# Optimization experiments

Measured on AMD Instinct MI355X. Metric: run time of the kernel, lower is better.

The kernel has to match this reference:

```python
import jax, jax.numpy as jnp
import numpy as np

N = 50000   # nodes
E = 800000  # edges
F = 128     # input features
H = 128     # hidden channels
G = 64      # graphs in batch
C = 10      # classes
L_HID = 3   # residual hidden GCN blocks
EPS = 1e-5  # BatchNorm eps


def setup_inputs() -> dict:
    key = jax.random.key(0)
    ks = jax.random.split(key, 10)
    sc = lambda k, s: (jax.random.normal(k, s, jnp.float32) * 0.05)
    x = jax.random.normal(ks[0], (N, F), jnp.float32)
    edge_index = jax.random.randint(ks[1], (2, E), 0, N, dtype=jnp.int32)
    batch = jnp.sort(jax.random.randint(ks[2], (N,), 0, G, dtype=jnp.int32))
    return {
        "x": x, "edge_index": edge_index, "batch": batch,
        # initial GCN block
        "W0": sc(ks[3], (F, H)), "b0": jnp.zeros(H, jnp.float32),
        "g0": jnp.ones(H, jnp.float32), "be0": jnp.zeros(H, jnp.float32),
        # 3 residual GCN blocks (stacked)
        "Wh": sc(ks[4], (L_HID, H, H)), "bh": jnp.zeros((L_HID, H), jnp.float32),
        "gh": jnp.ones((L_HID, H), jnp.float32), "beh": jnp.zeros((L_HID, H), jnp.float32),
        "Rh": sc(ks[5], (L_HID, H, H)),  # residual Linear (no bias)
        # MLP head: Linear(H,H)+ReLU, Linear(H,C)
        "mW1": sc(ks[6], (H, H)), "mb1": jnp.zeros(H, jnp.float32),
        "mW2": sc(ks[7], (H, C)), "mb2": jnp.zeros(C, jnp.float32),
    }


def _gcn_norm(edge_index, n):
    # add self-loops + symmetric normalization, as in PyG GCNConv
    loop = jnp.arange(n, dtype=edge_index.dtype)
    src = jnp.concatenate([edge_index[0], loop])
    dst = jnp.concatenate([edge_index[1], loop])
    deg = jax.ops.segment_sum(jnp.ones_like(dst, jnp.float32), dst, num_segments=n)
    dinv = jnp.where(deg > 0, jax.lax.rsqrt(deg), 0.0)
    coef = dinv[src] * dinv[dst]  # [E+N]
    return src, dst, coef


def _gcn_conv(x, W, b, src, dst, coef, n):
    h = x @ W                                   # [N, H] linear first (PyG order)
    msg = h[src] * coef[:, None]                # gather + normalize  [E+N, H]
    agg = jax.ops.segment_sum(msg, dst, num_segments=n)  # scatter-add [N, H]
    return agg + b


def _bn_relu(h, gamma, beta):
    # BatchNorm1d in eval mode with running_mean=0, running_var=1
    inv = jax.lax.rsqrt(jnp.asarray(1.0 + EPS, h.dtype))
    return jax.nn.relu(h * inv * gamma + beta)  # dropout is identity in eval


def reference(x, edge_index, batch, W0, b0, g0, be0, Wh, bh, gh, beh, Rh, mW1, mb1, mW2, mb2):
    n = x.shape[0]
    src, dst, coef = _gcn_norm(edge_index, n)
    # initial block (no residual)
    h = _bn_relu(_gcn_conv(x, W0, b0, src, dst, coef, n), g0, be0)
    # residual hidden blocks
    for i in range(Wh.shape[0]):
        c = _gcn_conv(h, Wh[i], bh[i], src, dst, coef, n) + h @ Rh[i]
        h = _bn_relu(c, gh[i], beh[i])
    # global max pool over graphs in the batch
    pooled = jax.ops.segment_max(h, batch, num_segments=G)  # [G, H]
    # MLP head
    z = jax.nn.relu(pooled @ mW1 + mb1)
    return z @ mW2 + mb2  # [G, C]
```

## Files before the change

kernel.cpp:

```cpp
#include <hip/hip_runtime.h>
#include <cstdint>
#include <cstddef>

#define NN 50000
#define NE 800000
#define NEPAD (NE + 3 * NN)
#define HID 128
#define NGRAPH 64
#define NCLASS 10
#define LHID 3
#define NREP 8

#define ROWBLK 3125
#define ROWBLK_PAD 3128
#define GEMM_GRID 782
#define FILL_GRID 3125
#define FRONT_DEG 3125
#define FRONT_A 3125
#define FRONT_B 56
#define FRONT_GRID (FRONT_DEG + FRONT_A + FRONT_B)

static constexpr float BN_INV = 0.9999950000374996f;

typedef __attribute__((ext_vector_type(8))) __bf16 bf16x8;
typedef __attribute__((ext_vector_type(4))) float floatx4;


__device__ __forceinline__ unsigned int f32_to_bf16_rne(float f) {
    unsigned int u = __float_as_uint(f);
    return (u + 0x7FFFu + ((u >> 16) & 1u)) >> 16;
}
__device__ __forceinline__ float bf16_to_f32(unsigned int h) {
    return __uint_as_float(h << 16);
}
__device__ __forceinline__ void split2(float a, float b, unsigned int& hi,
                                       unsigned int& lo) {
    unsigned int h0 = f32_to_bf16_rne(a), h1 = f32_to_bf16_rne(b);
    unsigned int l0 = f32_to_bf16_rne(a - bf16_to_f32(h0));
    unsigned int l1 = f32_to_bf16_rne(b - bf16_to_f32(h1));
    hi = h0 | (h1 << 16);
    lo = l0 | (l1 << 16);
}

__device__ __forceinline__ void gl2lds16(const void* g, void* l) {
    __builtin_amdgcn_global_load_lds((__attribute__((address_space(1))) void*)g,
                                     (__attribute__((address_space(3))) void*)l,
                                     16, 0, 0);
}


__global__ void k_front(const float* __restrict__ x, unsigned short* __restrict__ xH,
                        unsigned short* __restrict__ xL,
                        const float* __restrict__ W0, const float* __restrict__ Wh,
                        const float* __restrict__ Rh, unsigned short* __restrict__ bH,
                        unsigned short* __restrict__ bL,
                        const int* __restrict__ ei, int* __restrict__ deg8,
                        int* __restrict__ eslot) {
    const int b = blockIdx.x;
    const int tid = threadIdx.x;
    if (b < FRONT_DEG) {
        int e = b * 256 + tid;
        int d = ei[NE + e];
        int rep = e & (NREP - 1);
        eslot[e] = atomicAdd(&deg8[rep * NN + d], 1);
    } else if (b < FRONT_DEG + FRONT_A) {
        int u = (b - FRONT_DEG) * 256 + tid;
        int lane = u & 63;
        int blk = u >> 6;
        int kblk = blk & 3;
        int rowBlock = blk >> 2;
        int m = rowBlock * 16 + (lane & 15);
        int k = kblk * 32 + (lane >> 4) * 8;
        const float4* p = (const float4*)&x[(size_t)m * 128 + k];
        float4 v0 = p[0];
        float4 v1 = p[1];
        float vals[8] = {v0.x, v0.y, v0.z, v0.w, v1.x, v1.y, v1.z, v1.w};
        union { unsigned int i[4]; uint4 v; } H, L;
#pragma unroll
        for (int j = 0; j < 4; ++j) split2(vals[2 * j], vals[2 * j + 1], H.i[j], L.i[j]);
        *(uint4*)&xH[(size_t)u * 8] = H.v;
        *(uint4*)&xL[(size_t)u * 8] = L.v;
    } else {
        int cb = b - FRONT_DEG - FRONT_A;
        int mat = cb >> 3;
        const float* src = (mat == 0) ? W0
                         : (mat <= 3) ? (Wh + (size_t)(mat - 1) * 16384)
                                      : (Rh + (size_t)(mat - 4) * 16384);
        int u = (cb & 7) * 256 + tid;
        int lane = u & 63;
        int blk = u >> 6;
        int kblk = blk & 3;
        int nb = blk >> 2;
        int n = nb * 16 + (lane & 15);
        int k = kblk * 32 + (lane >> 4) * 8;
        union { unsigned int i[4]; uint4 v; } H, L;
#pragma unroll
        for (int j = 0; j < 4; ++j) {
            float a = src[(size_t)(k + 2 * j) * 128 + n];
            float c = src[(size_t)(k + 2 * j + 1) * 128 + n];
            split2(a, c, H.i[j], L.i[j]);
        }
        size_t base = (size_t)mat * 16384 + (size_t)u * 8;
        *(uint4*)&bH[base] = H.v;
        *(uint4*)&bL[base] = L.v;
    }
}


__global__ void k_scan1(const int* __restrict__ deg8, int* __restrict__ degT,
                        int* __restrict__ degOff, float* __restrict__ dinv,
                        int* __restrict__ bsum) {
    __shared__ int s[256];
    int i = blockIdx.x * 256 + threadIdx.x;
    int dsum = 0;
    if (i < NN) {
        int off[NREP];
#pragma unroll
        for (int r = 0; r < NREP; ++r) {
            off[r] = dsum;
            dsum += deg8[r * NN + i];
        }
#pragma unroll
        for (int r = 0; r < NREP; ++r) degOff[i * NREP + r] = off[r];
        degT[i] = dsum;
        dinv[i] = rsqrtf((float)(dsum + 1));
    }
    s[threadIdx.x] = (dsum + 3) & ~3;
    __syncthreads();
    for (int o = 128; o > 0; o >>= 1) {
        if (threadIdx.x < o) s[threadIdx.x] += s[threadIdx.x + o];
        __syncthreads();
    }
    if (threadIdx.x == 0) bsum[blockIdx.x] = s[0];
}


__global__ void k_scan3(const int* __restrict__ degT, const int* __restrict__ bsum,
                        int* __restrict__ rowptr, int* __restrict__ col,
                        float* __restrict__ cfv) {
    __shared__ int s[256];
    __shared__ int offS;
    const int bid = blockIdx.x;
    s[threadIdx.x] = (threadIdx.x < bid) ? bsum[threadIdx.x] : 0;
    __syncthreads();
    for (int o = 128; o > 0; o >>= 1) {
        if (threadIdx.x < o) s[threadIdx.x] += s[threadIdx.x + o];
        __syncthreads();
    }
    if (threadIdx.x == 0) offS = s[0];
    __syncthreads();
    const int off = offS;
    __syncthreads();
    int i = bid * 256 + threadIdx.x;
    int d = (i < NN) ? degT[i] : 0;
    int v = (d + 3) & ~3;
    s[threadIdx.x] = v;
    __syncthreads();
    for (int o = 1; o < 256; o <<= 1) {
        int tv = (threadIdx.x >= o) ? s[threadIdx.x - o] : 0;
        __syncthreads();
        s[threadIdx.x] += tv;
        __syncthreads();
    }
    if (i < NN) {
        int rp = off + s[threadIdx.x] - v;
        rowptr[i] = rp;
        for (int p = rp + d; p < rp + v; ++p) { col[p] = 0; cfv[p] = 0.f; }
    }
}


template <int NB, bool FILL>
__global__ __launch_bounds__(256, 3) void k_gemm_mfma(
    const unsigned short* __restrict__ Ahi, const unsigned short* __restrict__ Alo,
    const unsigned short* __restrict__ B1hi, const unsigned short* __restrict__ B1lo,
    const unsigned short* __restrict__ B2hi, const unsigned short* __restrict__ B2lo,
    float* __restrict__ C1, float* __restrict__ C2,
    const int* __restrict__ ei, const int* __restrict__ rowptr,
    const int* __restrict__ eslot, const int* __restrict__ degOff,
    const float* __restrict__ dinv, int* __restrict__ col,
    float* __restrict__ cfv) {
    __shared__ unsigned short lds[(1 + 2 * NB) * 4096];
    if (FILL && blockIdx.x >= GEMM_GRID) {
        int e = (blockIdx.x - GEMM_GRID) * 256 + threadIdx.x;
        int s = ei[e];
        int d = ei[NE + e];
        int rep = e & (NREP - 1);
        int p = rowptr[d] + degOff[d * NREP + rep] + eslot[e];
        col[p] = s;
        cfv[p] = dinv[s];
        return;
    }
    unsigned short* AhiS = lds;
    unsigned short* AloS = lds + 2048;
    unsigned short* B1hiS = lds + 4096;
    unsigned short* B1loS = lds + 8192;
    unsigned short* B2hiS = lds + 12288;
    unsigned short* B2loS = lds + 16384;

    const int tid = threadIdx.x;
    const int wave = tid >> 6;
    const int lane = tid & 63;
    const int wm = wave & 1;
    const int wn = wave >> 1;
    const int rb0 = blockIdx.x * 4;

    floatx4 acc1[2][4], acc2[2][4];
    floatx4 zero = {0.f, 0.f, 0.f, 0.f};
#pragma unroll
    for (int i = 0; i < 2; ++i)
#pragma unroll
        for (int j = 0; j < 4; ++j) { acc1[i][j] = zero; if (NB == 2) acc2[i][j] = zero; }

    for (int kc = 0; kc < 4; ++kc) {
        const int nit = (NB == 2) ? 10 : 6;
#pragma unroll
        for (int it = 0; it < nit; ++it) {
            int i = it * 4 + wave;
            const unsigned short* src;
            unsigned short* dst;
            if (i < 4)       { src = Ahi  + ((size_t)(rb0 + i) * 4 + kc) * 512;       dst = AhiS  + i * 512; }
            else if (i < 8)  { int rb = i - 4;  src = Alo  + ((size_t)(rb0 + rb) * 4 + kc) * 512; dst = AloS  + rb * 512; }
            else if (i < 16) { int nb = i - 8;  src = B1hi + ((size_t)nb * 4 + kc) * 512;         dst = B1hiS + nb * 512; }
            else if (i < 24) { int nb = i - 16; src = B1lo + ((size_t)nb * 4 + kc) * 512;         dst = B1loS + nb * 512; }
            else if (i < 32) { int nb = i - 24; src = B2hi + ((size_t)nb * 4 + kc) * 512;         dst = B2hiS + nb * 512; }
            else             { int nb = i - 32; src = B2lo + ((size_t)nb * 4 + kc) * 512;         dst = B2loS + nb * 512; }
            gl2lds16(src + (size_t)lane * 8, dst);
        }
        __syncthreads();

        bf16x8 aH[2], aL[2], bH[4], bL[4];
#pragma unroll
        for (int t = 0; t < 2; ++t)
            aH[t] = *(const bf16x8*)(AhiS + (wm * 2 + t) * 512 + lane * 8);
#pragma unroll
        for (int t = 0; t < 4; ++t)
            bH[t] = *(const bf16x8*)(B1hiS + (wn * 4 + t) * 512 + lane * 8);
#pragma unroll
        for (int tm = 0; tm < 2; ++tm)
#pragma unroll
            for (int tn = 0; tn < 4; ++tn)
                acc1[tm][tn] = __builtin_amdgcn_mfma_f32_16x16x32_bf16(
                    aH[tm], bH[tn], acc1[tm][tn], 0, 0, 0);
#pragma unroll
        for (int t = 0; t < 4; ++t)
            bL[t] = *(const bf16x8*)(B1loS + (wn * 4 + t) * 512 + lane * 8);
#pragma unroll
        for (int tm = 0; tm < 2; ++tm)
#pragma unroll
            for (int tn = 0; tn < 4; ++tn)
                acc1[tm][tn] = __builtin_amdgcn_mfma_f32_16x16x32_bf16(
                    aH[tm], bL[tn], acc1[tm][tn], 0, 0, 0);
#pragma unroll
        for (int t = 0; t < 2; ++t)
            aL[t] = *(const bf16x8*)(AloS + (wm * 2 + t) * 512 + lane * 8);
#pragma unroll
        for (int tm = 0; tm < 2; ++tm)
#pragma unroll
            for (int tn = 0; tn < 4; ++tn)
                acc1[tm][tn] = __builtin_amdgcn_mfma_f32_16x16x32_bf16(
                    aL[tm], bH[tn], acc1[tm][tn], 0, 0, 0);
        if (NB == 2) {
#pragma unroll
            for (int t = 0; t < 4; ++t)
                bH[t] = *(const bf16x8*)(B2hiS + (wn * 4 + t) * 512 + lane * 8);
#pragma unroll
            for (int tm = 0; tm < 2; ++tm)
#pragma unroll
                for (int tn = 0; tn < 4; ++tn)
                    acc2[tm][tn] = __builtin_amdgcn_mfma_f32_16x16x32_bf16(
                        aH[tm], bH[tn], acc2[tm][tn], 0, 0, 0);
#pragma unroll
            for (int tm = 0; tm < 2; ++tm)
#pragma unroll
                for (int tn = 0; tn < 4; ++tn)
                    acc2[tm][tn] = __builtin_amdgcn_mfma_f32_16x16x32_bf16(
                        aL[tm], bH[tn], acc2[tm][tn], 0, 0, 0);
#pragma unroll
            for (int t = 0; t < 4; ++t)
                bL[t] = *(const bf16x8*)(B2loS + (wn * 4 + t) * 512 + lane * 8);
#pragma unroll
            for (int tm = 0; tm < 2; ++tm)
#pragma unroll
                for (int tn = 0; tn < 4; ++tn)
                    acc2[tm][tn] = __builtin_amdgcn_mfma_f32_16x16x32_bf16(
                        aH[tm], bL[tn], acc2[tm][tn], 0, 0, 0);
        }
        __syncthreads();
    }

    const int quad = lane >> 4;
    const int col0 = lane & 15;
    const int rowBase = blockIdx.x * 64 + wm * 32;
#pragma unroll
    for (int tm = 0; tm < 2; ++tm) {
#pragma unroll
        for (int tn = 0; tn < 4; ++tn) {
            int c = wn * 64 + tn * 16 + col0;
#pragma unroll
            for (int r = 0; r < 4; ++r) {
                int row = rowBase + tm * 16 + quad * 4 + r;
                if (row < NN) {
                    C1[(size_t)row * 128 + c] = acc1[tm][tn][r];
                    if (NB == 2) C2[(size_t)row * 128 + c] = acc2[tm][tn][r];
                }
            }
        }
    }
}


template <bool RES, bool LAST>
__global__ __launch_bounds__(1024, 8) void k_spmm(
    const float* __restrict__ t, const float* __restrict__ r,
    const int* __restrict__ rowptr, const int* __restrict__ degT,
    const int* __restrict__ col, const float* __restrict__ cfv,
    const float* __restrict__ dinv, const float* __restrict__ bias,
    const float* __restrict__ gamma, const float* __restrict__ beta,
    unsigned short* __restrict__ hHi, unsigned short* __restrict__ hLo,
    const int* __restrict__ batch, float* __restrict__ pooled) {
    __shared__ unsigned short shH[16][136];
    __shared__ unsigned short shL[16][136];
    __shared__ float shP[16][128];
    const int tid = threadIdx.x;
    const int lane = tid & 63;
    const int h = lane >> 5;
    const int f4 = lane & 31;
    const int wv = __builtin_amdgcn_readfirstlane(tid >> 6);
    const int node = blockIdx.x * 16 + wv;

    const int start = __builtin_amdgcn_readfirstlane(rowptr[node]);
    const int cnt4 = __builtin_amdgcn_readfirstlane((degT[node] + 3) >> 2);

    float4 acc = {0.f, 0.f, 0.f, 0.f};
#pragma unroll 4
    for (int q = 0; q < cnt4; ++q) {
        const int4 cs = *(const int4*)(col + start + q * 4);
        const float4 wvv = *(const float4*)(cfv + start + q * 4);
        const int rowA = h ? cs.y : cs.x;
        const int rowB = h ? cs.w : cs.z;
        const float wA = h ? wvv.y : wvv.x;
        const float wB = h ? wvv.w : wvv.z;
        const float4 vA = *(const float4*)&t[(size_t)rowA * 128 + f4 * 4];
        const float4 vB = *(const float4*)&t[(size_t)rowB * 128 + f4 * 4];
        acc.x = fmaf(wA, vA.x, acc.x); acc.y = fmaf(wA, vA.y, acc.y);
        acc.z = fmaf(wA, vA.z, acc.z); acc.w = fmaf(wA, vA.w, acc.w);
        acc.x = fmaf(wB, vB.x, acc.x); acc.y = fmaf(wB, vB.y, acc.y);
        acc.z = fmaf(wB, vB.z, acc.z); acc.w = fmaf(wB, vB.w, acc.w);
    }
    acc.x += __shfl_xor(acc.x, 32);
    acc.y += __shfl_xor(acc.y, 32);
    acc.z += __shfl_xor(acc.z, 32);
    acc.w += __shfl_xor(acc.w, 32);

    const int f0 = f4 * 4;
    float4 o;
    if (h == 0) {
        const float di = dinv[node];
        const float dii = di * di;
        const float4 tv = *(const float4*)&t[(size_t)node * 128 + f0];
        const float4 bv = *(const float4*)&bias[f0];
        const float4 gv = *(const float4*)&gamma[f0];
        const float4 ev = *(const float4*)&beta[f0];
        float4 cc;
        cc.x = di * acc.x + dii * tv.x + bv.x;
        cc.y = di * acc.y + dii * tv.y + bv.y;
        cc.z = di * acc.z + dii * tv.z + bv.z;
        cc.w = di * acc.w + dii * tv.w + bv.w;
        if (RES) {
            const float4 rv = *(const float4*)&r[(size_t)node * 128 + f0];
            cc.x += rv.x; cc.y += rv.y; cc.z += rv.z; cc.w += rv.w;
        }
        o.x = fmaxf(cc.x * (BN_INV * gv.x) + ev.x, 0.f);
        o.y = fmaxf(cc.y * (BN_INV * gv.y) + ev.y, 0.f);
        o.z = fmaxf(cc.z * (BN_INV * gv.z) + ev.z, 0.f);
        o.w = fmaxf(cc.w * (BN_INV * gv.w) + ev.w, 0.f);
    }

    if (LAST) {
        bool uni = (batch[blockIdx.x * 16] == batch[blockIdx.x * 16 + 15]);
        if (uni) {
            if (h == 0) *(float4*)&shP[wv][f0] = o;
            __syncthreads();
            if (wv == 0) {
                float a = shP[0][2 * lane], b = shP[0][2 * lane + 1];
#pragma unroll
                for (int w = 1; w < 16; ++w) {
                    a = fmaxf(a, shP[w][2 * lane]);
                    b = fmaxf(b, shP[w][2 * lane + 1]);
                }
                int g = batch[blockIdx.x * 16];
                atomicMax((unsigned int*)&pooled[g * 128 + 2 * lane],
                          __float_as_uint(a));
                atomicMax((unsigned int*)&pooled[g * 128 + 2 * lane + 1],
                          __float_as_uint(b));
            }
        } else if (h == 0) {
            int g = batch[node];
            atomicMax((unsigned int*)&pooled[g * 128 + f0], __float_as_uint(o.x));
            atomicMax((unsigned int*)&pooled[g * 128 + f0 + 1], __float_as_uint(o.y));
            atomicMax((unsigned int*)&pooled[g * 128 + f0 + 2], __float_as_uint(o.z));
            atomicMax((unsigned int*)&pooled[g * 128 + f0 + 3], __float_as_uint(o.w));
        }
        return;
    }

    if (h == 0) {
        unsigned int H0, L0, H1, L1;
        split2(o.x, o.y, H0, L0);
        split2(o.z, o.w, H1, L1);
        ((unsigned int*)&shH[wv][0])[f4 * 2] = H0;
        ((unsigned int*)&shH[wv][0])[f4 * 2 + 1] = H1;
        ((unsigned int*)&shL[wv][0])[f4 * 2] = L0;
        ((unsigned int*)&shL[wv][0])[f4 * 2 + 1] = L1;
    }
    __syncthreads();

    const int u = tid >> 6;
    const int l = tid & 63;
    const int m = l & 15;
    const int kg = l >> 4;
    if (u < 4) {
        uint4 H4 = *(const uint4*)&shH[m][u * 32 + kg * 8];
        ((uint4*)hHi)[((size_t)blockIdx.x * 4 + u) * 64 + l] = H4;
    } else if (u < 8) {
        int uu = u - 4;
        uint4 L4 = *(const uint4*)&shL[m][uu * 32 + kg * 8];
        ((uint4*)hLo)[((size_t)blockIdx.x * 4 + uu) * 64 + l] = L4;
    }
}


__global__ void k_head(const float* __restrict__ pooled, const float* __restrict__ mW1,
                       const float* __restrict__ mb1, const float* __restrict__ mW2,
                       const float* __restrict__ mb2, float* __restrict__ out) {
    __shared__ float p[128];
    __shared__ float z[128];
    int g = blockIdx.x;
    int j = threadIdx.x;
    p[j] = pooled[g * 128 + j];
    __syncthreads();
    float a = mb1[j];
#pragma unroll 8
    for (int k = 0; k < 128; ++k) a += p[k] * mW1[k * 128 + j];
    z[j] = fmaxf(a, 0.f);
    __syncthreads();
    if (j < NCLASS) {
        float o = mb2[j];
#pragma unroll 8
        for (int k = 0; k < 128; ++k) o += z[k] * mW2[k * NCLASS + j];
        out[g * NCLASS + j] = o;
    }
}


extern "C" void kernel_launch(void* const* d_in, const int* in_sizes, int n_in,
                              void* d_out, int out_size, void* d_ws, size_t ws_size,
                              hipStream_t stream) {
    const float* x   = (const float*)d_in[0];
    const int*   ei  = (const int*)d_in[1];
    const int* batch = (const int*)d_in[2];
    const float* W0  = (const float*)d_in[3];
    const float* b0  = (const float*)d_in[4];
    const float* g0  = (const float*)d_in[5];
    const float* be0 = (const float*)d_in[6];
    const float* Wh  = (const float*)d_in[7];
    const float* bh  = (const float*)d_in[8];
    const float* gh  = (const float*)d_in[9];
    const float* beh = (const float*)d_in[10];
    const float* Rh  = (const float*)d_in[11];
    const float* mW1 = (const float*)d_in[12];
    const float* mb1 = (const float*)d_in[13];
    const float* mW2 = (const float*)d_in[14];
    const float* mb2 = (const float*)d_in[15];
    float* out = (float*)d_out;

    char* ws = (char*)d_ws;
    size_t off = 0;
    auto alloc = [&](size_t bytes) -> void* {
        void* p = ws + off;
        off += (bytes + 255) & ~(size_t)255;
        return p;
    };
    int*   deg8   = (int*)alloc((size_t)NREP * NN * 4);
    float* pooled = (float*)alloc((size_t)NGRAPH * HID * 4);
    size_t zspan = (size_t)((char*)pooled - (char*)deg8) + (size_t)NGRAPH * HID * 4;
    int*   degT   = (int*)alloc((size_t)NN * 4);
    int*   degOff = (int*)alloc((size_t)NN * NREP * 4);
    int*   rowptr = (int*)alloc((size_t)NN * 4);
    float* dinv   = (float*)alloc((size_t)NN * 4);
    int*   bsum   = (int*)alloc(256 * 4);
    int*   eslot  = (int*)alloc((size_t)NE * 4);
    int*   col    = (int*)alloc((size_t)NEPAD * 4);
    float* cfv    = (float*)alloc((size_t)NEPAD * 4);
    float* t      = (float*)alloc((size_t)NN * HID * 4);
    float* rbuf   = (float*)alloc((size_t)NN * HID * 4);
    const size_t ASZ = (size_t)ROWBLK_PAD * 4 * 512;
    unsigned short* xH = (unsigned short*)alloc(ASZ * 2);
    unsigned short* xL = (unsigned short*)alloc(ASZ * 2);
    unsigned short* hH0 = (unsigned short*)alloc(ASZ * 2);
    unsigned short* hL0 = (unsigned short*)alloc(ASZ * 2);
    unsigned short* hH1 = (unsigned short*)alloc(ASZ * 2);
    unsigned short* hL1 = (unsigned short*)alloc(ASZ * 2);
    unsigned short* bH = (unsigned short*)alloc((size_t)7 * 16384 * 2);
    unsigned short* bL = (unsigned short*)alloc((size_t)7 * 16384 * 2);

    hipMemsetAsync(deg8, 0, zspan, stream);

    k_front<<<FRONT_GRID, 256, 0, stream>>>(x, xH, xL, W0, Wh, Rh, bH, bL,
                                            ei, deg8, eslot);
    k_scan1<<<(NN + 255) / 256, 256, 0, stream>>>(deg8, degT, degOff, dinv, bsum);
    k_scan3<<<(NN + 255) / 256, 256, 0, stream>>>(degT, bsum, rowptr, col, cfv);

    k_gemm_mfma<1, true><<<GEMM_GRID + FILL_GRID, 256, 0, stream>>>(
        xH, xL, bH, bL, nullptr, nullptr, t, nullptr,
        ei, rowptr, eslot, degOff, dinv, col, cfv);

    const int spmmGrid = NN / 16;
    k_spmm<false, false><<<spmmGrid, 1024, 0, stream>>>(
        t, nullptr, rowptr, degT, col, cfv, dinv, b0, g0, be0, hH0, hL0,
        nullptr, nullptr);

    unsigned short* hh[2] = {hH0, hH1};
    unsigned short* hl[2] = {hL0, hL1};
    int cur = 0;
    for (int i = 0; i < LHID; ++i) {
        unsigned short* ih = hh[cur];
        unsigned short* il = hl[cur];
        unsigned short* oh = hh[cur ^ 1];
        unsigned short* ol = hl[cur ^ 1];
        const unsigned short* w1H = bH + (size_t)(1 + i) * 16384;
        const unsigned short* w1L = bL + (size_t)(1 + i) * 16384;
        const unsigned short* w2H = bH + (size_t)(4 + i) * 16384;
        const unsigned short* w2L = bL + (size_t)(4 + i) * 16384;
        k_gemm_mfma<2, false><<<GEMM_GRID, 256, 0, stream>>>(
            ih, il, w1H, w1L, w2H, w2L, t, rbuf,
            nullptr, nullptr, nullptr, nullptr, nullptr, nullptr, nullptr);
        if (i < LHID - 1)
            k_spmm<true, false><<<spmmGrid, 1024, 0, stream>>>(
                t, rbuf, rowptr, degT, col, cfv, dinv, bh + i * HID, gh + i * HID,
                beh + i * HID, oh, ol, nullptr, nullptr);
        else
            k_spmm<true, true><<<spmmGrid, 1024, 0, stream>>>(
                t, rbuf, rowptr, degT, col, cfv, dinv, bh + i * HID, gh + i * HID,
                beh + i * HID, nullptr, nullptr, batch, pooled);
        cur ^= 1;
    }

    k_head<<<NGRAPH, 128, 0, stream>>>(pooled, mW1, mb1, mW2, mb2, out);
}
```

Before: 497.6 us.

## Fuse x bf16 split into first GEMM and load operands directly to registers

The separate pass that converts x into hi/lo bf16 tiles in the front kernel is removed. The first GEMM now reads fp32 x and splits it in registers. Separately, the GEMM drops its LDS staging and block barriers, loading A and B fragments straight from global memory into registers. This saves the x round-trip through memory and the sync overhead, at the cost of redundant global reads of B across waves and no shared-memory reuse.

```diff
diff --git a/kernel.cpp b/kernel.cpp
--- a/kernel.cpp
+++ b/kernel.cpp
@@ -16,9 +16,8 @@
 #define GEMM_GRID 782
 #define FILL_GRID 3125
 #define FRONT_DEG 3125
-#define FRONT_A 3125
 #define FRONT_B 56
-#define FRONT_GRID (FRONT_DEG + FRONT_A + FRONT_B)
+#define FRONT_GRID (FRONT_DEG + FRONT_B)
 
 static constexpr float BN_INV = 0.9999950000374996f;
 
@@ -42,16 +41,8 @@
     lo = l0 | (l1 << 16);
 }
 
-__device__ __forceinline__ void gl2lds16(const void* g, void* l) {
-    __builtin_amdgcn_global_load_lds((__attribute__((address_space(1))) void*)g,
-                                     (__attribute__((address_space(3))) void*)l,
-                                     16, 0, 0);
-}
-
-
-__global__ void k_front(const float* __restrict__ x, unsigned short* __restrict__ xH,
-                        unsigned short* __restrict__ xL,
-                        const float* __restrict__ W0, const float* __restrict__ Wh,
+
+__global__ void k_front(const float* __restrict__ W0, const float* __restrict__ Wh,
                         const float* __restrict__ Rh, unsigned short* __restrict__ bH,
                         unsigned short* __restrict__ bL,
                         const int* __restrict__ ei, int* __restrict__ deg8,
@@ -63,25 +54,8 @@
         int d = ei[NE + e];
         int rep = e & (NREP - 1);
         eslot[e] = atomicAdd(&deg8[rep * NN + d], 1);
-    } else if (b < FRONT_DEG + FRONT_A) {
-        int u = (b - FRONT_DEG) * 256 + tid;
-        int lane = u & 63;
-        int blk = u >> 6;
-        int kblk = blk & 3;
-        int rowBlock = blk >> 2;
-        int m = rowBlock * 16 + (lane & 15);
-        int k = kblk * 32 + (lane >> 4) * 8;
-        const float4* p = (const float4*)&x[(size_t)m * 128 + k];
-        float4 v0 = p[0];
-        float4 v1 = p[1];
-        float vals[8] = {v0.x, v0.y, v0.z, v0.w, v1.x, v1.y, v1.z, v1.w};
-        union { unsigned int i[4]; uint4 v; } H, L;
-#pragma unroll
-        for (int j = 0; j < 4; ++j) split2(vals[2 * j], vals[2 * j + 1], H.i[j], L.i[j]);
-        *(uint4*)&xH[(size_t)u * 8] = H.v;
-        *(uint4*)&xL[(size_t)u * 8] = L.v;
     } else {
-        int cb = b - FRONT_DEG - FRONT_A;
+        int cb = b - FRONT_DEG;
         int mat = cb >> 3;
         const float* src = (mat == 0) ? W0
                          : (mat <= 3) ? (Wh + (size_t)(mat - 1) * 16384)
@@ -170,8 +144,9 @@
 }
 
 
-template <int NB, bool FILL>
+template <int NB, bool FILL, bool XA>
 __global__ __launch_bounds__(256, 3) void k_gemm_mfma(
+    const float* __restrict__ X,
     const unsigned short* __restrict__ Ahi, const unsigned short* __restrict__ Alo,
     const unsigned short* __restrict__ B1hi, const unsigned short* __restrict__ B1lo,
     const unsigned short* __restrict__ B2hi, const unsigned short* __restrict__ B2lo,
@@ -180,7 +155,6 @@
     const int* __restrict__ eslot, const int* __restrict__ degOff,
     const float* __restrict__ dinv, int* __restrict__ col,
     float* __restrict__ cfv) {
-    __shared__ unsigned short lds[(1 + 2 * NB) * 4096];
     if (FILL && blockIdx.x >= GEMM_GRID) {
         int e = (blockIdx.x - GEMM_GRID) * 256 + threadIdx.x;
         int s = ei[e];
@@ -191,13 +165,6 @@
         cfv[p] = dinv[s];
         return;
     }
-    unsigned short* AhiS = lds;
-    unsigned short* AloS = lds + 2048;
-    unsigned short* B1hiS = lds + 4096;
-    unsigned short* B1loS = lds + 8192;
-    unsigned short* B2hiS = lds + 12288;
-    unsigned short* B2loS = lds + 16384;
-
     const int tid = threadIdx.x;
     const int wave = tid >> 6;
     const int lane = tid & 63;
@@ -212,30 +179,38 @@
 #pragma unroll
         for (int j = 0; j < 4; ++j) { acc1[i][j] = zero; if (NB == 2) acc2[i][j] = zero; }
 
+#pragma unroll
     for (int kc = 0; kc < 4; ++kc) {
-        const int nit = (NB == 2) ? 10 : 6;
-#pragma unroll
-        for (int it = 0; it < nit; ++it) {
-            int i = it * 4 + wave;
-            const unsigned short* src;
-            unsigned short* dst;
-            if (i < 4)       { src = Ahi  + ((size_t)(rb0 + i) * 4 + kc) * 512;       dst = AhiS  + i * 512; }
-            else if (i < 8)  { int rb = i - 4;  src = Alo  + ((size_t)(rb0 + rb) * 4 + kc) * 512; dst = AloS  + rb * 512; }
-            else if (i < 16) { int nb = i - 8;  src = B1hi + ((size_t)nb * 4 + kc) * 512;         dst = B1hiS + nb * 512; }
-            else if (i < 24) { int nb = i - 16; src = B1lo + ((size_t)nb * 4 + kc) * 512;         dst = B1loS + nb * 512; }
-            else if (i < 32) { int nb = i - 24; src = B2hi + ((size_t)nb * 4 + kc) * 512;         dst = B2hiS + nb * 512; }
-            else             { int nb = i - 32; src = B2lo + ((size_t)nb * 4 + kc) * 512;         dst = B2loS + nb * 512; }
-            gl2lds16(src + (size_t)lane * 8, dst);
-        }
-        __syncthreads();
-
         bf16x8 aH[2], aL[2], bH[4], bL[4];
-#pragma unroll
-        for (int t = 0; t < 2; ++t)
-            aH[t] = *(const bf16x8*)(AhiS + (wm * 2 + t) * 512 + lane * 8);
+        if (XA) {
+#pragma unroll
+            for (int t = 0; t < 2; ++t) {
+                int m = (rb0 + wm * 2 + t) * 16 + (lane & 15);
+                if (m >= NN) m = NN - 1;
+                const float4* p =
+                    (const float4*)&X[(size_t)m * 128 + kc * 32 + (lane >> 4) * 8];
+                float4 v0 = p[0];
+                float4 v1 = p[1];
+                float vals[8] = {v0.x, v0.y, v0.z, v0.w, v1.x, v1.y, v1.z, v1.w};
+                union { unsigned int i[4]; bf16x8 v; } H, L;
+#pragma unroll
+                for (int j = 0; j < 4; ++j)
+                    split2(vals[2 * j], vals[2 * j + 1], H.i[j], L.i[j]);
+                aH[t] = H.v;
+                aL[t] = L.v;
+            }
+        } else {
+#pragma unroll
+            for (int t = 0; t < 2; ++t) {
+                size_t u = ((size_t)(rb0 + wm * 2 + t) * 4 + kc) * 512 + lane * 8;
+                aH[t] = *(const bf16x8*)(Ahi + u);
+                aL[t] = *(const bf16x8*)(Alo + u);
+            }
+        }
 #pragma unroll
         for (int t = 0; t < 4; ++t)
-            bH[t] = *(const bf16x8*)(B1hiS + (wn * 4 + t) * 512 + lane * 8);
+            bH[t] = *(const bf16x8*)(B1hi + ((size_t)(wn * 4 + t) * 4 + kc) * 512 +
+                                     lane * 8);
 #pragma unroll
         for (int tm = 0; tm < 2; ++tm)
 #pragma unroll
@@ -244,16 +219,14 @@
                     aH[tm], bH[tn], acc1[tm][tn], 0, 0, 0);
 #pragma unroll
         for (int t = 0; t < 4; ++t)
-            bL[t] = *(const bf16x8*)(B1loS + (wn * 4 + t) * 512 + lane * 8);
+            bL[t] = *(const bf16x8*)(B1lo + ((size_t)(wn * 4 + t) * 4 + kc) * 512 +
+                                     lane * 8);
 #pragma unroll
         for (int tm = 0; tm < 2; ++tm)
 #pragma unroll
             for (int tn = 0; tn < 4; ++tn)
                 acc1[tm][tn] = __builtin_amdgcn_mfma_f32_16x16x32_bf16(
                     aH[tm], bL[tn], acc1[tm][tn], 0, 0, 0);
-#pragma unroll
-        for (int t = 0; t < 2; ++t)
-            aL[t] = *(const bf16x8*)(AloS + (wm * 2 + t) * 512 + lane * 8);
 #pragma unroll
         for (int tm = 0; tm < 2; ++tm)
 #pragma unroll
@@ -263,7 +236,8 @@
         if (NB == 2) {
 #pragma unroll
             for (int t = 0; t < 4; ++t)
-                bH[t] = *(const bf16x8*)(B2hiS + (wn * 4 + t) * 512 + lane * 8);
+                bH[t] = *(const bf16x8*)(B2hi + ((size_t)(wn * 4 + t) * 4 + kc) * 512 +
+                                         lane * 8);
 #pragma unroll
             for (int tm = 0; tm < 2; ++tm)
 #pragma unroll
@@ -278,7 +252,8 @@
                         aL[tm], bH[tn], acc2[tm][tn], 0, 0, 0);
 #pragma unroll
             for (int t = 0; t < 4; ++t)
-                bL[t] = *(const bf16x8*)(B2loS + (wn * 4 + t) * 512 + lane * 8);
+                bL[t] = *(const bf16x8*)(B2lo + ((size_t)(wn * 4 + t) * 4 + kc) * 512 +
+                                         lane * 8);
 #pragma unroll
             for (int tm = 0; tm < 2; ++tm)
 #pragma unroll
@@ -286,7 +261,6 @@
                     acc2[tm][tn] = __builtin_amdgcn_mfma_f32_16x16x32_bf16(
                         aH[tm], bL[tn], acc2[tm][tn], 0, 0, 0);
         }
-        __syncthreads();
     }
 
     const int quad = lane >> 4;
@@ -496,8 +470,6 @@
     float* t      = (float*)alloc((size_t)NN * HID * 4);
     float* rbuf   = (float*)alloc((size_t)NN * HID * 4);
     const size_t ASZ = (size_t)ROWBLK_PAD * 4 * 512;
-    unsigned short* xH = (unsigned short*)alloc(ASZ * 2);
-    unsigned short* xL = (unsigned short*)alloc(ASZ * 2);
     unsigned short* hH0 = (unsigned short*)alloc(ASZ * 2);
     unsigned short* hL0 = (unsigned short*)alloc(ASZ * 2);
     unsigned short* hH1 = (unsigned short*)alloc(ASZ * 2);
@@ -507,13 +479,12 @@
 
     hipMemsetAsync(deg8, 0, zspan, stream);
 
-    k_front<<<FRONT_GRID, 256, 0, stream>>>(x, xH, xL, W0, Wh, Rh, bH, bL,
-                                            ei, deg8, eslot);
+    k_front<<<FRONT_GRID, 256, 0, stream>>>(W0, Wh, Rh, bH, bL, ei, deg8, eslot);
     k_scan1<<<(NN + 255) / 256, 256, 0, stream>>>(deg8, degT, degOff, dinv, bsum);
     k_scan3<<<(NN + 255) / 256, 256, 0, stream>>>(degT, bsum, rowptr, col, cfv);
 
-    k_gemm_mfma<1, true><<<GEMM_GRID + FILL_GRID, 256, 0, stream>>>(
-        xH, xL, bH, bL, nullptr, nullptr, t, nullptr,
+    k_gemm_mfma<1, true, true><<<GEMM_GRID + FILL_GRID, 256, 0, stream>>>(
+        x, nullptr, nullptr, bH, bL, nullptr, nullptr, t, nullptr,
         ei, rowptr, eslot, degOff, dinv, col, cfv);
 
     const int spmmGrid = NN / 16;
@@ -533,8 +504,8 @@
         const unsigned short* w1L = bL + (size_t)(1 + i) * 16384;
         const unsigned short* w2H = bH + (size_t)(4 + i) * 16384;
         const unsigned short* w2L = bL + (size_t)(4 + i) * 16384;
-        k_gemm_mfma<2, false><<<GEMM_GRID, 256, 0, stream>>>(
-            ih, il, w1H, w1L, w2H, w2L, t, rbuf,
+        k_gemm_mfma<2, false, false><<<GEMM_GRID, 256, 0, stream>>>(
+            nullptr, ih, il, w1H, w1L, w2H, w2L, t, rbuf,
             nullptr, nullptr, nullptr, nullptr, nullptr, nullptr, nullptr);
         if (i < LHID - 1)
             k_spmm<true, false><<<spmmGrid, 1024, 0, stream>>>(
```

After: 502.2 us. About the same (+0.9%).
